# Kernel optimization log

Measured on AMD Instinct MI355X. Metric: run time of the kernel, lower is better.

The kernel has to match this reference:

```python
import jax, jax.numpy as jnp
import numpy as np
import math

B, S, D = 4, 2048, 1024
H = 16
DH = D // H  # 64
DFF = 4096
EPS = 1e-5


def layernorm(x, g, b):
    mu = jnp.mean(x, axis=-1, keepdims=True)
    var = jnp.var(x, axis=-1, keepdims=True)
    return (x - mu) * jax.lax.rsqrt(var + EPS) * g + b


def setup_inputs() -> dict:
    key = jax.random.key(0)
    ks = jax.random.split(key, 16)
    s = 0.02
    return {
        "src": jax.random.normal(ks[0], (B, S, D), jnp.float32),
        # per-head q/k/v projections stacked: [H, D, DH]
        "Wq": jax.random.normal(ks[1], (H, D, DH), jnp.float32) * s,
        "bq": jnp.zeros((H, DH), jnp.float32),
        "Wk": jax.random.normal(ks[2], (H, D, DH), jnp.float32) * s,
        "bk": jnp.zeros((H, DH), jnp.float32),
        "Wv": jax.random.normal(ks[3], (H, D, DH), jnp.float32) * s,
        "bv": jnp.zeros((H, DH), jnp.float32),
        "Wo": jax.random.normal(ks[4], (D, D), jnp.float32) * s,
        "bo": jnp.zeros((D,), jnp.float32),
        "ln1_g": jnp.ones((D,), jnp.float32),
        "ln1_b": jnp.zeros((D,), jnp.float32),
        "W1": jax.random.normal(ks[5], (D, DFF), jnp.float32) * s,
        "b1": jnp.zeros((DFF,), jnp.float32),
        "W2": jax.random.normal(ks[6], (DFF, D), jnp.float32) * s,
        "b2": jnp.zeros((D,), jnp.float32),
        "ln2_g": jnp.ones((D,), jnp.float32),
        "ln2_b": jnp.zeros((D,), jnp.float32),
    }


def reference(src, Wq, bq, Wk, bk, Wv, bv, Wo, bo, ln1_g, ln1_b,
              W1, b1, W2, b2, ln2_g, ln2_b):
    # Batched equivalent of the per-head Python loop (no causal mask: mask=False)
    q = jnp.einsum('bsd,hde->bhse', src, Wq) + bq[None, :, None, :]
    k = jnp.einsum('bsd,hde->bhse', src, Wk) + bk[None, :, None, :]
    v = jnp.einsum('bsd,hde->bhse', src, Wv) + bv[None, :, None, :]
    scores = jnp.einsum('bhse,bhte->bhst', q, k) / math.sqrt(DH)
    attn = jax.nn.softmax(scores, axis=-1)
    ctx = jnp.einsum('bhst,bhte->bhse', attn, v)  # [B,H,S,DH]
    # cat over heads on last dim == transpose then merge
    ctx = ctx.transpose(0, 2, 1, 3).reshape(B, S, D)
    attn_out = ctx @ Wo + bo
    x1 = layernorm(attn_out + src, ln1_g, ln1_b)
    ffn = jax.nn.relu(x1 @ W1 + b1) @ W2 + b2
    return layernorm(ffn + x1, ln2_g, ln2_b)
```

## Files before the change

kernel.cpp:

```cpp
#include <hip/hip_runtime.h>
#include <stdint.h>

#define DEV __device__ __forceinline__

typedef float f32x4 __attribute__((ext_vector_type(4)));
typedef __bf16 bf16x8 __attribute__((ext_vector_type(8)));
typedef unsigned short u16x4 __attribute__((ext_vector_type(4)));
typedef unsigned short u16x8 __attribute__((ext_vector_type(8)));

DEV unsigned short f2bf(float f) {
  unsigned u = __builtin_bit_cast(unsigned, f);
  u += 0x7fffu + ((u >> 16) & 1u);
  return (unsigned short)(u >> 16);
}
DEV float bf2f(unsigned short h) {
  unsigned u = ((unsigned)h) << 16;
  return __builtin_bit_cast(float, u);
}
DEV void gload_lds16(const void* g, void* l) {
  __builtin_amdgcn_global_load_lds((const __attribute__((address_space(1))) void*)g,
                                   (__attribute__((address_space(3))) void*)l, 16, 0, 0);
}

__global__ void cvt_f32_bf16(const float* __restrict__ in, unsigned short* __restrict__ out, int n) {
  int i = (blockIdx.x * 256 + threadIdx.x) * 4;
  if (i >= n) return;
  f32x4 v = *(const f32x4*)(in + i);
  u16x4 o;
  o[0] = f2bf(v[0]); o[1] = f2bf(v[1]); o[2] = f2bf(v[2]); o[3] = f2bf(v[3]);
  *(u16x4*)(out + i) = o;
}

__global__ void transpose_cvt(const float* __restrict__ src, unsigned short* __restrict__ dst,
                              int R, int C) {
  __shared__ __align__(16) float t[64][65];
  const int tid = threadIdx.x;
  const int r0 = blockIdx.x * 64, c0 = blockIdx.y * 64;
  const int rr = tid >> 2, q = tid & 3;
  const float* s = src + (size_t)(r0 + rr) * C + c0 + q * 16;
#pragma unroll
  for (int j = 0; j < 4; ++j) {
    f32x4 v = *(const f32x4*)(s + j * 4);
    t[rr][q * 16 + j * 4 + 0] = v[0];
    t[rr][q * 16 + j * 4 + 1] = v[1];
    t[rr][q * 16 + j * 4 + 2] = v[2];
    t[rr][q * 16 + j * 4 + 3] = v[3];
  }
  __syncthreads();
  const int cc = tid >> 2, qq = tid & 3;
  unsigned short* o = dst + (size_t)(c0 + cc) * R + r0 + qq * 16;
  u16x8 a, b;
#pragma unroll
  for (int j = 0; j < 8; ++j) {
    a[j] = f2bf(t[qq * 16 + j][cc]);
    b[j] = f2bf(t[qq * 16 + 8 + j][cc]);
  }
  *(u16x8*)o = a;
  *(u16x8*)(o + 8) = b;
}

__global__ void pack_qkv_w(const float* __restrict__ Wq, const float* __restrict__ Wk,
                           const float* __restrict__ Wv, unsigned short* __restrict__ dst) {
  __shared__ __align__(16) float t[64][65];
  const int tid = threadIdx.x;
  const int z = blockIdx.z, part = z >> 4, h = z & 15;
  const float* src = (part == 0 ? Wq : (part == 1 ? Wk : Wv)) + (size_t)h * 65536;
  const int r0 = blockIdx.x * 64;
  const int rr = tid >> 2, q = tid & 3;
  const float* s = src + (size_t)(r0 + rr) * 64 + q * 16;
#pragma unroll
  for (int j = 0; j < 4; ++j) {
    f32x4 v = *(const f32x4*)(s + j * 4);
    t[rr][q * 16 + j * 4 + 0] = v[0];
    t[rr][q * 16 + j * 4 + 1] = v[1];
    t[rr][q * 16 + j * 4 + 2] = v[2];
    t[rr][q * 16 + j * 4 + 3] = v[3];
  }
  __syncthreads();
  const int cc = tid >> 2, qq = tid & 3;
  unsigned short* o = dst + ((size_t)(part * 1024 + h * 64 + cc)) * 1024 + r0 + qq * 16;
  u16x8 a, b;
#pragma unroll
  for (int j = 0; j < 8; ++j) {
    a[j] = f2bf(t[qq * 16 + j][cc]);
    b[j] = f2bf(t[qq * 16 + 8 + j][cc]);
  }
  *(u16x8*)o = a;
  *(u16x8*)(o + 8) = b;
}

__global__ void pack_bias(const float* __restrict__ bq, const float* __restrict__ bk,
                          const float* __restrict__ bv, float* __restrict__ o) {
  int i = blockIdx.x * 256 + threadIdx.x;
  o[i] = i < 1024 ? bq[i] : (i < 2048 ? bk[i - 1024] : bv[i - 2048]);
}

__global__ void vtrans(const unsigned short* __restrict__ v, unsigned short* __restrict__ vt) {
  __shared__ __align__(16) unsigned short t[64][72];
  const int tid = threadIdx.x;
  const int bh = blockIdx.y, s0 = blockIdx.x * 64;
  const int r = tid >> 2, q = (tid & 3) * 16;
  const unsigned short* g = v + ((size_t)bh * 2048 + s0 + r) * 64 + q;
  *(u16x8*)&t[r][q] = *(const u16x8*)g;
  *(u16x8*)&t[r][q + 8] = *(const u16x8*)(g + 8);
  __syncthreads();
  const int d = tid >> 2, qq = (tid & 3) * 16;
  unsigned short* o = vt + ((size_t)bh * 64 + d) * 2048 + s0 + qq;
  u16x8 a, b;
#pragma unroll
  for (int j = 0; j < 8; ++j) {
    a[j] = t[qq + j][d];
    b[j] = t[qq + 8 + j][d];
  }
  *(u16x8*)o = a;
  *(u16x8*)(o + 8) = b;
}

template <int MODE>
__global__ __launch_bounds__(256, 2) void gemm_bt(
    const unsigned short* __restrict__ A, const unsigned short* __restrict__ Bt,
    const float* __restrict__ bias, unsigned short* __restrict__ out,
    unsigned short* __restrict__ qb, unsigned short* __restrict__ kb,
    unsigned short* __restrict__ vb, int M, int N, int K) {
  __shared__ __align__(16) char As[16384];
  __shared__ __align__(16) char Bs[16384];
  const int tid = threadIdx.x;
  const int wave = tid >> 6, lane = tid & 63;
  const int lrow = lane & 15;
  const int kof = (lane >> 4) * 16;
  const int m0 = blockIdx.y * 128, n0 = blockIdx.x * 128;
  const int wm = (wave >> 1) * 64, wn = (wave & 1) * 64;
  const int chunkrow = lane >> 3;
  const int colb0 = (lane & 7) * 16;

  f32x4 acc[4][4] = {};

  for (int k0 = 0; k0 < K; k0 += 64) {
#pragma unroll
    for (int c = 0; c < 4; ++c) {
      const int chunk = wave * 4 + c;
      const int rowA = chunk * 8 + chunkrow;
      const int srcb = colb0 ^ ((rowA & 7) << 4);
      const char* ga = (const char*)A + ((size_t)(m0 + rowA) * K + k0) * 2 + srcb;
      const char* gb = (const char*)Bt + ((size_t)(n0 + rowA) * K + k0) * 2 + srcb;
      gload_lds16(ga, As + chunk * 1024);
      gload_lds16(gb, Bs + chunk * 1024);
    }
    __syncthreads();
#pragma unroll
    for (int kk = 0; kk < 2; ++kk) {
      bf16x8 af[4], bv4[4];
#pragma unroll
      for (int i = 0; i < 4; ++i) {
        const int ra = wm + i * 16 + lrow;
        af[i] = *(const bf16x8*)(As + ra * 128 + ((kk * 64 + kof) ^ ((ra & 7) << 4)));
        const int rb = wn + i * 16 + lrow;
        bv4[i] = *(const bf16x8*)(Bs + rb * 128 + ((kk * 64 + kof) ^ ((rb & 7) << 4)));
      }
#pragma unroll
      for (int mi = 0; mi < 4; ++mi)
#pragma unroll
        for (int ni = 0; ni < 4; ++ni)
          acc[mi][ni] = __builtin_amdgcn_mfma_f32_16x16x32_bf16(af[mi], bv4[ni], acc[mi][ni], 0, 0, 0);
    }
    __syncthreads();
  }

#pragma unroll
  for (int mi = 0; mi < 4; ++mi) {
    const int row = m0 + wm + mi * 16 + ((lane >> 4) << 2);
#pragma unroll
    for (int ni = 0; ni < 4; ++ni) {
      const int col = n0 + wn + ni * 16 + lrow;
      const float bvv = bias[col];
#pragma unroll
      for (int r = 0; r < 4; ++r) {
        float v = acc[mi][ni][r] + bvv;
        if (MODE == 1) v = fmaxf(v, 0.0f);
        const int rr = row + r;
        if constexpr (MODE == 2) {
          const int part = col >> 10, cc = col & 1023, h = cc >> 6, e = cc & 63;
          unsigned short* dst = part == 0 ? qb : (part == 1 ? kb : vb);
          dst[(((size_t)((rr >> 11) * 16 + h)) * 2048 + (rr & 2047)) * 64 + e] = f2bf(v);
        } else {
          out[(size_t)rr * N + col] = f2bf(v);
        }
      }
    }
  }
}

__global__ __launch_bounds__(256, 2) void attn_kernel(
    const unsigned short* __restrict__ q_buf, const unsigned short* __restrict__ k_buf,
    const unsigned short* __restrict__ vt_buf, unsigned short* __restrict__ ctx) {
  __shared__ __align__(16) unsigned short Ks[64][72];
  __shared__ __align__(16) unsigned short Vs[64][72];
  __shared__ __align__(16) unsigned short Ps[4][32][72];
  const int tid = threadIdx.x, wave = tid >> 6, lane = tid & 63;
  const int bh = blockIdx.y;
  const int q0 = blockIdx.x * 128;
  const int lrow = lane & 15, lg = lane >> 4;
  const int kofs = lg * 8;

  bf16x8 qf[2][2];
#pragma unroll
  for (int mt = 0; mt < 2; ++mt)
#pragma unroll
    for (int kk = 0; kk < 2; ++kk)
      qf[mt][kk] = *(const bf16x8*)(q_buf +
          ((size_t)bh * 2048 + q0 + wave * 32 + mt * 16 + lrow) * 64 + kk * 32 + kofs);

  f32x4 acc_o[2][4] = {};
  float l_reg[2][4] = {};

  const int stg_r = tid >> 2;
  const int stg_p = (tid & 3) * 16;

  for (int t = 0; t < 32; ++t) {
    const int kt0 = t * 64;
    {
      const unsigned short* gk = k_buf + ((size_t)bh * 2048 + kt0 + stg_r) * 64 + stg_p;
      u16x8 a = *(const u16x8*)gk, b = *(const u16x8*)(gk + 8);
      *(u16x8*)&Ks[stg_r][stg_p] = a;
      *(u16x8*)&Ks[stg_r][stg_p + 8] = b;
      const unsigned short* gv = vt_buf + ((size_t)bh * 64 + stg_r) * 2048 + kt0 + stg_p;
      u16x8 c = *(const u16x8*)gv, d = *(const u16x8*)(gv + 8);
      *(u16x8*)&Vs[stg_r][stg_p] = c;
      *(u16x8*)&Vs[stg_r][stg_p + 8] = d;
    }
    __syncthreads();

    f32x4 sacc[2][4] = {};
#pragma unroll
    for (int kk = 0; kk < 2; ++kk) {
      bf16x8 bfr[4];
#pragma unroll
      for (int nt = 0; nt < 4; ++nt)
        bfr[nt] = *(const bf16x8*)&Ks[nt * 16 + lrow][kk * 32 + kofs];
#pragma unroll
      for (int mt = 0; mt < 2; ++mt)
#pragma unroll
        for (int nt = 0; nt < 4; ++nt)
          sacc[mt][nt] = __builtin_amdgcn_mfma_f32_16x16x32_bf16(qf[mt][kk], bfr[nt], sacc[mt][nt], 0, 0, 0);
    }

#pragma unroll
    for (int mt = 0; mt < 2; ++mt)
#pragma unroll
      for (int r = 0; r < 4; ++r) {
        const int ql = mt * 16 + lg * 4 + r;
        float p0 = __expf(sacc[mt][0][r] * 0.125f);
        float p1 = __expf(sacc[mt][1][r] * 0.125f);
        float p2 = __expf(sacc[mt][2][r] * 0.125f);
        float p3 = __expf(sacc[mt][3][r] * 0.125f);
        Ps[wave][ql][0 + lrow] = f2bf(p0);
        Ps[wave][ql][16 + lrow] = f2bf(p1);
        Ps[wave][ql][32 + lrow] = f2bf(p2);
        Ps[wave][ql][48 + lrow] = f2bf(p3);
        float ps = (p0 + p1) + (p2 + p3);
        ps += __shfl_xor(ps, 1);
        ps += __shfl_xor(ps, 2);
        ps += __shfl_xor(ps, 4);
        ps += __shfl_xor(ps, 8);
        l_reg[mt][r] += ps;
      }
    __syncthreads();

#pragma unroll
    for (int kk = 0; kk < 2; ++kk) {
      bf16x8 pfr[2], vfr[4];
#pragma unroll
      for (int mt = 0; mt < 2; ++mt)
        pfr[mt] = *(const bf16x8*)&Ps[wave][mt * 16 + lrow][kk * 32 + kofs];
#pragma unroll
      for (int nd = 0; nd < 4; ++nd)
        vfr[nd] = *(const bf16x8*)&Vs[nd * 16 + lrow][kk * 32 + kofs];
#pragma unroll
      for (int mt = 0; mt < 2; ++mt)
#pragma unroll
        for (int nd = 0; nd < 4; ++nd)
          acc_o[mt][nd] = __builtin_amdgcn_mfma_f32_16x16x32_bf16(pfr[mt], vfr[nd], acc_o[mt][nd], 0, 0, 0);
    }
    __syncthreads();
  }

  const int b = bh >> 4, h = bh & 15;
#pragma unroll
  for (int mt = 0; mt < 2; ++mt)
#pragma unroll
    for (int r = 0; r < 4; ++r) {
      const float inv = 1.0f / l_reg[mt][r];
      const int s = q0 + wave * 32 + mt * 16 + lg * 4 + r;
#pragma unroll
      for (int nd = 0; nd < 4; ++nd)
        ctx[((size_t)(b * 2048 + s)) * 1024 + h * 64 + nd * 16 + lrow] =
            f2bf(acc_o[mt][nd][r] * inv);
    }
}

template <bool RES_BF, bool OUT_F32>
__global__ __launch_bounds__(256) void ln_kernel(
    const unsigned short* __restrict__ xin, const void* __restrict__ res,
    const float* __restrict__ g, const float* __restrict__ b, void* __restrict__ out) {
  const int row = blockIdx.x, tid = threadIdx.x;
  const size_t base = (size_t)row * 1024 + tid * 4;
  float x[4];
  u16x4 xv = *(const u16x4*)(xin + base);
  if constexpr (RES_BF) {
    u16x4 rv = *(const u16x4*)((const unsigned short*)res + base);
#pragma unroll
    for (int j = 0; j < 4; ++j) x[j] = bf2f(xv[j]) + bf2f(rv[j]);
  } else {
    f32x4 rv = *(const f32x4*)((const float*)res + base);
#pragma unroll
    for (int j = 0; j < 4; ++j) x[j] = bf2f(xv[j]) + rv[j];
  }
  float s1 = 0.f, s2 = 0.f;
#pragma unroll
  for (int j = 0; j < 4; ++j) { s1 += x[j]; s2 += x[j] * x[j]; }
#pragma unroll
  for (int off = 32; off > 0; off >>= 1) {
    s1 += __shfl_down(s1, off);
    s2 += __shfl_down(s2, off);
  }
  __shared__ float red[8];
  const int wv = tid >> 6, ln = tid & 63;
  if (ln == 0) { red[wv] = s1; red[4 + wv] = s2; }
  __syncthreads();
  s1 = red[0] + red[1] + red[2] + red[3];
  s2 = red[4] + red[5] + red[6] + red[7];
  const float mu = s1 * (1.0f / 1024.0f);
  const float rs = rsqrtf(s2 * (1.0f / 1024.0f) - mu * mu + 1e-5f);
#pragma unroll
  for (int j = 0; j < 4; ++j) {
    const float y = (x[j] - mu) * rs * g[tid * 4 + j] + b[tid * 4 + j];
    if constexpr (OUT_F32) ((float*)out)[base + j] = y;
    else ((unsigned short*)out)[base + j] = f2bf(y);
  }
}

static const size_t OFF_SBF  = 0;
static const size_t OFF_Q    = 16777216;
static const size_t OFF_K    = 33554432;
static const size_t OFF_V    = 50331648;
static const size_t OFF_VT   = 67108864;
static const size_t OFF_WQKV = 83886080;
static const size_t OFF_BQKV = 90177536;
static const size_t OFF_WO   = 90189824;
static const size_t OFF_W1   = 92286976;
static const size_t OFF_W2   = 100675584;
static const size_t OFF_CTX  = 109064192;
static const size_t OFF_AO   = 125841408;
static const size_t OFF_X1   = 142618624;
static const size_t OFF_FFN  = 159395840;

extern "C" void kernel_launch(void* const* d_in, const int* in_sizes, int n_in,
                              void* d_out, int out_size, void* d_ws, size_t ws_size,
                              hipStream_t stream) {
  const float* src = (const float*)d_in[0];
  const float* Wq  = (const float*)d_in[1];
  const float* bq  = (const float*)d_in[2];
  const float* Wk  = (const float*)d_in[3];
  const float* bk  = (const float*)d_in[4];
  const float* Wv  = (const float*)d_in[5];
  const float* bv  = (const float*)d_in[6];
  const float* Wo  = (const float*)d_in[7];
  const float* bo  = (const float*)d_in[8];
  const float* g1  = (const float*)d_in[9];
  const float* be1 = (const float*)d_in[10];
  const float* W1  = (const float*)d_in[11];
  const float* b1  = (const float*)d_in[12];
  const float* W2  = (const float*)d_in[13];
  const float* b2  = (const float*)d_in[14];
  const float* g2  = (const float*)d_in[15];
  const float* be2 = (const float*)d_in[16];

  char* ws = (char*)d_ws;
  unsigned short* sbf  = (unsigned short*)(ws + OFF_SBF);
  unsigned short* h1   = (unsigned short*)(ws + OFF_SBF);
  unsigned short* qb   = (unsigned short*)(ws + OFF_Q);
  unsigned short* kb   = (unsigned short*)(ws + OFF_K);
  unsigned short* vb   = (unsigned short*)(ws + OFF_V);
  unsigned short* vtb  = (unsigned short*)(ws + OFF_VT);
  unsigned short* wqkv = (unsigned short*)(ws + OFF_WQKV);
  float*          bqkv = (float*)(ws + OFF_BQKV);
  unsigned short* wot  = (unsigned short*)(ws + OFF_WO);
  unsigned short* w1t  = (unsigned short*)(ws + OFF_W1);
  unsigned short* w2t  = (unsigned short*)(ws + OFF_W2);
  unsigned short* ctx  = (unsigned short*)(ws + OFF_CTX);
  unsigned short* ao   = (unsigned short*)(ws + OFF_AO);
  unsigned short* x1   = (unsigned short*)(ws + OFF_X1);
  unsigned short* ffn  = (unsigned short*)(ws + OFF_FFN);
  float* outp = (float*)d_out;

  cvt_f32_bf16<<<dim3(8192), dim3(256), 0, stream>>>(src, sbf, 8388608);
  pack_qkv_w<<<dim3(16, 1, 48), dim3(256), 0, stream>>>(Wq, Wk, Wv, wqkv);
  pack_bias<<<dim3(12), dim3(256), 0, stream>>>(bq, bk, bv, bqkv);
  transpose_cvt<<<dim3(16, 16), dim3(256), 0, stream>>>(Wo, wot, 1024, 1024);
  transpose_cvt<<<dim3(16, 64), dim3(256), 0, stream>>>(W1, w1t, 1024, 4096);
  transpose_cvt<<<dim3(64, 16), dim3(256), 0, stream>>>(W2, w2t, 4096, 1024);

  gemm_bt<2><<<dim3(24, 64), dim3(256), 0, stream>>>(sbf, wqkv, bqkv, nullptr, qb, kb, vb,
                                                     8192, 3072, 1024);
  vtrans<<<dim3(32, 64), dim3(256), 0, stream>>>(vb, vtb);
  attn_kernel<<<dim3(16, 64), dim3(256), 0, stream>>>(qb, kb, vtb, ctx);
  gemm_bt<0><<<dim3(8, 64), dim3(256), 0, stream>>>(ctx, wot, bo, ao, nullptr, nullptr, nullptr,
                                                    8192, 1024, 1024);
  ln_kernel<false, false><<<dim3(8192), dim3(256), 0, stream>>>(ao, src, g1, be1, x1);
  gemm_bt<1><<<dim3(32, 64), dim3(256), 0, stream>>>(x1, w1t, b1, h1, nullptr, nullptr, nullptr,
                                                     8192, 4096, 1024);
  gemm_bt<0><<<dim3(8, 64), dim3(256), 0, stream>>>(h1, w2t, b2, ffn, nullptr, nullptr, nullptr,
                                                    8192, 1024, 4096);
  ln_kernel<true, true><<<dim3(8192), dim3(256), 0, stream>>>(ffn, x1, g2, be2, outp);

  (void)in_sizes; (void)n_in; (void)out_size; (void)ws_size;
}
```

Baseline: 427.6 us.

## Double-buffer attention K/V via direct LDS loads and compute row sums with MFMA

Rewrites the attention inner loop so K/V tiles are double-buffered with global_load_lds into XOR-swizzled LDS, removing one barrier per iteration and overlapping the next tile's load with compute. The softmax scale and log2(e) are folded into Q in the QKV GEMM epilogue so exp2f can be used directly. The row-sum shuffle reduction is replaced by an extra MFMA against a ones vector. It also remaps the grid so consecutive blocks cover different heads, raises the occupancy hint to 3, and adds setprio around the MFMA groups. The row sum now accumulates bf16-rounded P values, which changes numerics slightly.

```diff
diff --git a/kernel.cpp b/kernel.cpp
--- a/kernel.cpp
+++ b/kernel.cpp
@@ -180,6 +180,7 @@
         const int rr = row + r;
         if constexpr (MODE == 2) {
           const int part = col >> 10, cc = col & 1023, h = cc >> 6, e = cc & 63;
+          if (part == 0) v *= 0.18033688011112042f;
           unsigned short* dst = part == 0 ? qb : (part == 1 ? kb : vb);
           dst[(((size_t)((rr >> 11) * 16 + h)) * 2048 + (rr & 2047)) * 64 + e] = f2bf(v);
         } else {
@@ -190,17 +191,17 @@
   }
 }
 
-__global__ __launch_bounds__(256, 2) void attn_kernel(
+__global__ __launch_bounds__(256, 3) void attn_kernel(
     const unsigned short* __restrict__ q_buf, const unsigned short* __restrict__ k_buf,
     const unsigned short* __restrict__ vt_buf, unsigned short* __restrict__ ctx) {
-  __shared__ __align__(16) unsigned short Ks[64][72];
-  __shared__ __align__(16) unsigned short Vs[64][72];
-  __shared__ __align__(16) unsigned short Ps[4][32][72];
+  __shared__ __align__(16) char Ks[2][8192];
+  __shared__ __align__(16) char Vs[2][8192];
+  __shared__ __align__(16) __bf16 Ps[4][32][72];
   const int tid = threadIdx.x, wave = tid >> 6, lane = tid & 63;
-  const int bh = blockIdx.y;
-  const int q0 = blockIdx.x * 128;
+  const int wg = (blockIdx.x & 7) * 128 + (blockIdx.x >> 3);
+  const int bh = wg >> 4;
+  const int q0 = (wg & 15) * 128;
   const int lrow = lane & 15, lg = lane >> 4;
-  const int kofs = lg * 8;
 
   bf16x8 qf[2][2];
 #pragma unroll
@@ -208,40 +209,49 @@
 #pragma unroll
     for (int kk = 0; kk < 2; ++kk)
       qf[mt][kk] = *(const bf16x8*)(q_buf +
-          ((size_t)bh * 2048 + q0 + wave * 32 + mt * 16 + lrow) * 64 + kk * 32 + kofs);
+          ((size_t)bh * 2048 + q0 + wave * 32 + mt * 16 + lrow) * 64 + kk * 32 + lg * 8);
 
   f32x4 acc_o[2][4] = {};
-  float l_reg[2][4] = {};
-
-  const int stg_r = tid >> 2;
-  const int stg_p = (tid & 3) * 16;
-
+  f32x4 accd[2] = {};
+  bf16x8 ones;
+#pragma unroll
+  for (int j = 0; j < 8; ++j) ones[j] = (lrow == 0) ? (__bf16)1.0f : (__bf16)0.0f;
+
+  auto stage = [&](int t, int buf) {
+#pragma unroll
+    for (int i = 0; i < 2; ++i) {
+      const int c = i * 256 + wave * 64 + lane;
+      const int row = c >> 3;
+      const int col = ((c & 7) * 16) ^ ((row & 7) << 4);
+      gload_lds16((const char*)k_buf + ((size_t)(bh * 2048 + t * 64 + row)) * 128 + col,
+                  &Ks[buf][(i * 256 + wave * 64) * 16]);
+      gload_lds16((const char*)vt_buf + ((size_t)(bh * 64 + row)) * 4096 + t * 128 + col,
+                  &Vs[buf][(i * 256 + wave * 64) * 16]);
+    }
+  };
+
+  stage(0, 0);
   for (int t = 0; t < 32; ++t) {
-    const int kt0 = t * 64;
-    {
-      const unsigned short* gk = k_buf + ((size_t)bh * 2048 + kt0 + stg_r) * 64 + stg_p;
-      u16x8 a = *(const u16x8*)gk, b = *(const u16x8*)(gk + 8);
-      *(u16x8*)&Ks[stg_r][stg_p] = a;
-      *(u16x8*)&Ks[stg_r][stg_p + 8] = b;
-      const unsigned short* gv = vt_buf + ((size_t)bh * 64 + stg_r) * 2048 + kt0 + stg_p;
-      u16x8 c = *(const u16x8*)gv, d = *(const u16x8*)(gv + 8);
-      *(u16x8*)&Vs[stg_r][stg_p] = c;
-      *(u16x8*)&Vs[stg_r][stg_p + 8] = d;
-    }
+    const int cur = t & 1;
     __syncthreads();
+    stage(t < 31 ? t + 1 : 31, cur ^ 1);
 
     f32x4 sacc[2][4] = {};
 #pragma unroll
     for (int kk = 0; kk < 2; ++kk) {
       bf16x8 bfr[4];
 #pragma unroll
-      for (int nt = 0; nt < 4; ++nt)
-        bfr[nt] = *(const bf16x8*)&Ks[nt * 16 + lrow][kk * 32 + kofs];
+      for (int nt = 0; nt < 4; ++nt) {
+        const int row = nt * 16 + lrow;
+        bfr[nt] = *(const bf16x8*)&Ks[cur][row * 128 + ((kk * 64 + lg * 16) ^ ((row & 7) << 4))];
+      }
+      __builtin_amdgcn_s_setprio(1);
 #pragma unroll
       for (int mt = 0; mt < 2; ++mt)
 #pragma unroll
         for (int nt = 0; nt < 4; ++nt)
           sacc[mt][nt] = __builtin_amdgcn_mfma_f32_16x16x32_bf16(qf[mt][kk], bfr[nt], sacc[mt][nt], 0, 0, 0);
+      __builtin_amdgcn_s_setprio(0);
     }
 
 #pragma unroll
@@ -249,39 +259,32 @@
 #pragma unroll
       for (int r = 0; r < 4; ++r) {
         const int ql = mt * 16 + lg * 4 + r;
-        float p0 = __expf(sacc[mt][0][r] * 0.125f);
-        float p1 = __expf(sacc[mt][1][r] * 0.125f);
-        float p2 = __expf(sacc[mt][2][r] * 0.125f);
-        float p3 = __expf(sacc[mt][3][r] * 0.125f);
-        Ps[wave][ql][0 + lrow] = f2bf(p0);
-        Ps[wave][ql][16 + lrow] = f2bf(p1);
-        Ps[wave][ql][32 + lrow] = f2bf(p2);
-        Ps[wave][ql][48 + lrow] = f2bf(p3);
-        float ps = (p0 + p1) + (p2 + p3);
-        ps += __shfl_xor(ps, 1);
-        ps += __shfl_xor(ps, 2);
-        ps += __shfl_xor(ps, 4);
-        ps += __shfl_xor(ps, 8);
-        l_reg[mt][r] += ps;
-      }
-    __syncthreads();
+#pragma unroll
+        for (int nt = 0; nt < 4; ++nt)
+          Ps[wave][ql][nt * 16 + lrow] = (__bf16)exp2f(sacc[mt][nt][r]);
+      }
 
 #pragma unroll
     for (int kk = 0; kk < 2; ++kk) {
       bf16x8 pfr[2], vfr[4];
 #pragma unroll
       for (int mt = 0; mt < 2; ++mt)
-        pfr[mt] = *(const bf16x8*)&Ps[wave][mt * 16 + lrow][kk * 32 + kofs];
-#pragma unroll
-      for (int nd = 0; nd < 4; ++nd)
-        vfr[nd] = *(const bf16x8*)&Vs[nd * 16 + lrow][kk * 32 + kofs];
-#pragma unroll
-      for (int mt = 0; mt < 2; ++mt)
+        pfr[mt] = *(const bf16x8*)&Ps[wave][mt * 16 + lrow][kk * 32 + lg * 8];
+#pragma unroll
+      for (int nd = 0; nd < 4; ++nd) {
+        const int row = nd * 16 + lrow;
+        vfr[nd] = *(const bf16x8*)&Vs[cur][row * 128 + ((kk * 64 + lg * 16) ^ ((row & 7) << 4))];
+      }
+      __builtin_amdgcn_s_setprio(1);
+#pragma unroll
+      for (int mt = 0; mt < 2; ++mt) {
+        accd[mt] = __builtin_amdgcn_mfma_f32_16x16x32_bf16(pfr[mt], ones, accd[mt], 0, 0, 0);
 #pragma unroll
         for (int nd = 0; nd < 4; ++nd)
           acc_o[mt][nd] = __builtin_amdgcn_mfma_f32_16x16x32_bf16(pfr[mt], vfr[nd], acc_o[mt][nd], 0, 0, 0);
-    }
-    __syncthreads();
+      }
+      __builtin_amdgcn_s_setprio(0);
+    }
   }
 
   const int b = bh >> 4, h = bh & 15;
@@ -289,7 +292,8 @@
   for (int mt = 0; mt < 2; ++mt)
 #pragma unroll
     for (int r = 0; r < 4; ++r) {
-      const float inv = 1.0f / l_reg[mt][r];
+      const float den = __shfl(accd[mt][r], lane & 48);
+      const float inv = 1.0f / den;
       const int s = q0 + wave * 32 + mt * 16 + lg * 4 + r;
 #pragma unroll
       for (int nd = 0; nd < 4; ++nd)
@@ -403,7 +407,7 @@
   gemm_bt<2><<<dim3(24, 64), dim3(256), 0, stream>>>(sbf, wqkv, bqkv, nullptr, qb, kb, vb,
                                                      8192, 3072, 1024);
   vtrans<<<dim3(32, 64), dim3(256), 0, stream>>>(vb, vtb);
-  attn_kernel<<<dim3(16, 64), dim3(256), 0, stream>>>(qb, kb, vtb, ctx);
+  attn_kernel<<<dim3(1024), dim3(256), 0, stream>>>(qb, kb, vtb, ctx);
   gemm_bt<0><<<dim3(8, 64), dim3(256), 0, stream>>>(ctx, wot, bo, ao, nullptr, nullptr, nullptr,
                                                     8192, 1024, 1024);
   ln_kernel<false, false><<<dim3(8192), dim3(256), 0, stream>>>(ao, src, g1, be1, x1);
```

Result: faster. 398.9 us (-6.7%).
